# Performance work log

Hardware: AMD Instinct MI355X
Metric: run time of the kernel (lower is better)

The kernel has to match this reference:

```python
import jax, jax.numpy as jnp
import numpy as np

V, E, M, L = 32000, 1024, 4096, 4  # vocab, embed_dim, mlp_dim, mlp_layers
B, S = 4, 2048                      # batch, seq_len


def setup_inputs() -> dict:
    key = jax.random.key(0)
    ks = jax.random.split(key, 7)
    init = lambda k, shape, fan: (jax.random.normal(k, shape, jnp.float32) / np.sqrt(fan).astype(np.float32))
    return {
        "x": jax.random.randint(ks[0], (B, S), 0, V),
        "emb": init(ks[1], (V, E), E),
        "Wq": init(ks[2], (E, E), E), "bq": jnp.zeros((E,), jnp.float32),
        "Wk": init(ks[3], (E, E), E), "bk": jnp.zeros((E,), jnp.float32),
        "Wv": init(ks[4], (E, E), E), "bv": jnp.zeros((E,), jnp.float32),
        "W1": init(ks[5], (L, E, M), E), "b1": jnp.zeros((L, M), jnp.float32),
        "W2": init(ks[6], (L, M, E), M), "b2": jnp.zeros((L, E), jnp.float32),
    }


def reference(x, emb, Wq, bq, Wk, bk, Wv, bv, W1, b1, W2, b2):
    h = emb[x]                                   # [B,S,E]
    q = h @ Wq + bq
    k = h @ Wk + bk
    v = h @ Wv + bv
    scale = 1.0 / np.sqrt(E).astype(np.float32)
    scores = jnp.einsum("bse,bte->bst", q, k) * scale   # [B,S,S]
    # torch.triu(ones, diagonal=0): keep upper triangle incl. diagonal (anti-causal/suffix mask)
    mask = jnp.triu(jnp.ones((S, S), dtype=bool), k=0)
    scores = jnp.where(mask, scores, -jnp.inf)
    w = jax.nn.softmax(scores, axis=-1)
    h = jax.nn.relu(jnp.einsum("bst,bte->bse", w, v))
    for i in range(L):
        h = jax.nn.relu(h @ W1[i] + b1[i])
        h = jax.nn.relu(h @ W2[i] + b2[i])
    return h
```

## Files before the change

### kernel.cpp

```cpp
#include <hip/hip_runtime.h>
#include <hip/hip_bf16.h>

#define EDIM 1024
#define MDIM 4096
#define SEQ  2048
#define NB   4
#define ROWS 8192

typedef short bh8 __attribute__((ext_vector_type(8)));
typedef float f32x16 __attribute__((ext_vector_type(16)));

__device__ __forceinline__ float bf2f(unsigned short u) {
    return __uint_as_float(((unsigned int)u) << 16);
}
__device__ __forceinline__ unsigned short f2bf(float f) {
    unsigned int u = __float_as_uint(f);
    u += 0x7FFFu + ((u >> 16) & 1u);
    return (unsigned short)(u >> 16);
}
__device__ __forceinline__ void splitf(float v, unsigned short& h, unsigned short& l) {
    h = f2bf(v);
    l = f2bf(v - __uint_as_float(((unsigned int)h) << 16));
}
__device__ __forceinline__ void ld4f(const float* __restrict__ p, float* d) {
    const float4 v = *reinterpret_cast<const float4*>(p);
    d[0] = v.x; d[1] = v.y; d[2] = v.z; d[3] = v.w;
}
__device__ __forceinline__ void ld4h(const unsigned short* __restrict__ p, float* d) {
    const ushort4 v = *reinterpret_cast<const ushort4*>(p);
    d[0] = bf2f(v.x); d[1] = bf2f(v.y); d[2] = bf2f(v.z); d[3] = bf2f(v.w);
}

__device__ __forceinline__ long long tidx8(int n, int k, int KD16) {
    return ((((long long)(n >> 5) * KD16 + (k >> 4)) * 2 + ((k >> 3) & 1)) * 32 + (n & 31)) * 8;
}

__global__ __launch_bounds__(64)
void sniff_k(const unsigned int* __restrict__ w, int* __restrict__ flag) {
    int ok = 0;
    const int base = threadIdx.x * 32;
#pragma unroll
    for (int i = 0; i < 32; ++i) {
        const unsigned int v = w[base + i];
        const unsigned int lo = v & 0xFFFFu, hi = v >> 16;
        const unsigned int el = (lo >> 7) & 0xFF, eh = (hi >> 7) & 0xFF;
        const bool okl = (lo == 0u) || (el >= 0x30u && el <= 0x7Eu);
        const bool okh = (hi == 0u) || (eh >= 0x30u && eh <= 0x7Eu);
        ok += (okl && okh) ? 1 : 0;
    }
#pragma unroll
    for (int off = 32; off > 0; off >>= 1) ok += __shfl_down(ok, off);
    if (threadIdx.x == 0) *flag = (ok > 1400) ? 1 : 0;
}

__global__ __launch_bounds__(256)
void gather_k(const int* __restrict__ x, const void* __restrict__ emb,
              unsigned short* __restrict__ oh, unsigned short* __restrict__ ol,
              const int* __restrict__ flagp) {
    const int bf = *flagp;
    const int row = blockIdx.x;
    const int idx = x[row];
    const int k = threadIdx.x * 4;
    const long long off = (long long)idx * EDIM + k;
    float d[4];
    if (bf) ld4h((const unsigned short*)emb + off, d);
    else    ld4f((const float*)emb + off, d);
    unsigned short h0, l0, h1, l1, h2, l2, h3, l3;
    splitf(d[0], h0, l0); splitf(d[1], h1, l1);
    splitf(d[2], h2, l2); splitf(d[3], h3, l3);
    const long long o = (((long long)(row >> 5) * 64 + (k >> 4)) * 2 + ((k >> 3) & 1)) * 256
                        + (row & 31) * 8 + (k & 7);
    *reinterpret_cast<ushort4*>(oh + o) = make_ushort4(h0, h1, h2, h3);
    *reinterpret_cast<ushort4*>(ol + o) = make_ushort4(l0, l1, l2, l3);
}

__global__ __launch_bounds__(256)
void splitT_tiled_k(const void* __restrict__ in, unsigned short* __restrict__ oh,
                    unsigned short* __restrict__ ol, int Kd, int Nd,
                    long long inOff, const int* __restrict__ flagp, int bF) {
    const int bf = bF ? *flagp : 0;
    const int k0 = blockIdx.y * 32, n0 = blockIdx.x * 32;
    const int KD16 = Kd >> 4;
    __shared__ float t[32][33];
    const int c = threadIdx.x & 31, r0 = threadIdx.x >> 5;
#pragma unroll
    for (int i = 0; i < 4; ++i) {
        const int r = r0 + i * 8;
        const long long off = inOff + (long long)(k0 + r) * Nd + n0 + c;
        t[r][c] = bf ? bf2f(((const unsigned short*)in)[off]) : ((const float*)in)[off];
    }
    __syncthreads();
#pragma unroll
    for (int i = 0; i < 4; ++i) {
        const int r = r0 + i * 8;
        const float v = t[c][r];
        unsigned short hh, ll;
        splitf(v, hh, ll);
        const int n = n0 + r, k = k0 + c;
        const long long oo = tidx8(n, k, KD16) + (k & 7);
        oh[oo] = hh; ol[oo] = ll;
    }
}

template<int OM, bool BIAS, bool RELU, bool MASK>
__global__ __launch_bounds__(256, 3)
void mgemm_k(const unsigned short* __restrict__ Ah,
             const unsigned short* __restrict__ Al,
             const unsigned short* __restrict__ Bh,
             const unsigned short* __restrict__ Bl,
             const void* __restrict__ biasv,
             void* __restrict__ Cv, void* __restrict__ Cv2,
             int M, int N, int K,
             long long sA, long long sB, long long sC,
             long long biasBase, float scale, int oKD16, long long zOut, int rowMul,
             const int* __restrict__ flagp, int bF, int cF) {
    const int flag = *flagp;
    const int bfBias = bF ? flag : 0;
    const int bfC = cF ? flag : 0;

    Ah += (long long)blockIdx.z * sA;
    Al += (long long)blockIdx.z * sA;
    Bh += (long long)blockIdx.z * sB;
    Bl += (long long)blockIdx.z * sB;
    const long long zC = (long long)blockIdx.z * sC;
    const int rowOff = rowMul * blockIdx.z;

    const int GX = gridDim.x;
    const int f = blockIdx.y * GX + blockIdx.x;
    const int gxpc = GX >> 3;
    const int xcd = f & 7, p = f >> 3;
    const int bx = xcd * gxpc + (p % gxpc);
    const int by = p / gxpc;
    const int brow = by * 128, bcol = bx * 128;

    const int tid = threadIdx.x;
    const int lane = tid & 63, wave = tid >> 6;
    const int wr = wave >> 1, wc = wave & 1;
    const int l31 = lane & 31, lhi = lane >> 5;

    if (MASK && (bcol + 127 < brow)) {
#pragma unroll
        for (int mi = 0; mi < 2; ++mi) {
            const int rbase = brow + wr * 64 + mi * 32 + 4 * lhi;
#pragma unroll
            for (int ni = 0; ni < 2; ++ni) {
                const int c = bcol + wc * 64 + ni * 32 + l31;
#pragma unroll
                for (int e = 0; e < 16; ++e) {
                    const int r = rbase + (e & 3) + 8 * (e >> 2);
                    ((float*)Cv)[zC + (long long)r * N + c] = -1e30f;
                }
            }
        }
        return;
    }

    const int KD16 = K >> 4;

    const long long aoff0 = ((long long)((brow >> 5) + wr * 2 + 0) * KD16) * 512 + lane * 8;
    const long long aoff1 = aoff0 + (long long)KD16 * 512;
    const long long boff0 = ((long long)((bcol >> 5) + wc * 2 + 0) * KD16) * 512 + lane * 8;
    const long long boff1 = boff0 + (long long)KD16 * 512;

    const unsigned short* __restrict__ pAh0 = Ah + aoff0;
    const unsigned short* __restrict__ pAh1 = Ah + aoff1;
    const unsigned short* __restrict__ pAl0 = Al + aoff0;
    const unsigned short* __restrict__ pAl1 = Al + aoff1;
    const unsigned short* __restrict__ pBh0 = Bh + boff0;
    const unsigned short* __restrict__ pBh1 = Bh + boff1;
    const unsigned short* __restrict__ pBl0 = Bl + boff0;
    const unsigned short* __restrict__ pBl1 = Bl + boff1;

    f32x16 acc00, acc01, acc10, acc11;
#pragma unroll
    for (int e = 0; e < 16; ++e) { acc00[e] = 0.f; acc01[e] = 0.f; acc10[e] = 0.f; acc11[e] = 0.f; }

    bh8 p_ah0, p_ah1, p_al0, p_al1, p_bh0, p_bh1, p_bl0, p_bl1;
    bh8 q_ah0, q_ah1, q_al0, q_al1, q_bh0, q_bh1, q_bl0, q_bl1;

#define MFMA_(d, a, b) d = __builtin_amdgcn_mfma_f32_32x32x16_bf16(a, b, d, 0, 0, 0)

#define LOADSET(S, J) { \
    const long long o_ = (long long)(J) * 512; \
    S##ah0 = *reinterpret_cast<const bh8*>(pAh0 + o_); \
    S##ah1 = *reinterpret_cast<const bh8*>(pAh1 + o_); \
    S##al0 = *reinterpret_cast<const bh8*>(pAl0 + o_); \
    S##al1 = *reinterpret_cast<const bh8*>(pAl1 + o_); \
    S##bh0 = *reinterpret_cast<const bh8*>(pBh0 + o_); \
    S##bh1 = *reinterpret_cast<const bh8*>(pBh1 + o_); \
    S##bl0 = *reinterpret_cast<const bh8*>(pBl0 + o_); \
    S##bl1 = *reinterpret_cast<const bh8*>(pBl1 + o_); }

#define COMPSET(S) { \
    MFMA_(acc00, S##ah0, S##bh0); MFMA_(acc01, S##ah0, S##bh1); \
    MFMA_(acc10, S##ah1, S##bh0); MFMA_(acc11, S##ah1, S##bh1); \
    MFMA_(acc00, S##ah0, S##bl0); MFMA_(acc01, S##ah0, S##bl1); \
    MFMA_(acc10, S##ah1, S##bl0); MFMA_(acc11, S##ah1, S##bl1); \
    MFMA_(acc00, S##al0, S##bh0); MFMA_(acc01, S##al0, S##bh1); \
    MFMA_(acc10, S##al1, S##bh0); MFMA_(acc11, S##al1, S##bh1); }

    LOADSET(p_, 0);
    LOADSET(q_, 1);

    for (int j = 0; j + 3 < KD16; j += 2) {
        if ((j & 7) == 6) __builtin_amdgcn_s_barrier();
        __builtin_amdgcn_s_setprio(1);
        COMPSET(p_);
        __builtin_amdgcn_s_setprio(0);
        LOADSET(p_, j + 2);
        __builtin_amdgcn_s_setprio(1);
        COMPSET(q_);
        __builtin_amdgcn_s_setprio(0);
        LOADSET(q_, j + 3);
    }
    COMPSET(p_);
    COMPSET(q_);

#undef LOADSET
#undef COMPSET
#undef MFMA_

    const f32x16* accp[4] = {&acc00, &acc01, &acc10, &acc11};

#pragma unroll
    for (int mi = 0; mi < 2; ++mi) {
        const int rbase = brow + wr * 64 + mi * 32 + 4 * lhi;
#pragma unroll
        for (int ni = 0; ni < 2; ++ni) {
            const f32x16& a = *accp[mi * 2 + ni];
            const int c = bcol + wc * 64 + ni * 32 + l31;
            float bv = 0.f;
            if (BIAS) {
                const long long bo = biasBase + c;
                bv = bfBias ? bf2f(((const unsigned short*)biasv)[bo])
                            : ((const float*)biasv)[bo];
            }
            if constexpr (OM == 3) {
#pragma unroll
                for (int g = 0; g < 4; ++g) {
                    const int t0 = rbase + 8 * g;
                    const int z = t0 >> 11, tt = t0 & 2047;
                    float vv[4];
#pragma unroll
                    for (int d = 0; d < 4; ++d) {
                        float v = a[g * 4 + d];
                        if (BIAS) v += bv;
                        if (RELU) v = fmaxf(v, 0.f);
                        vv[d] = v;
                    }
                    unsigned short h0, l0, h1, l1, h2, l2, h3, l3;
                    splitf(vv[0], h0, l0); splitf(vv[1], h1, l1);
                    splitf(vv[2], h2, l2); splitf(vv[3], h3, l3);
                    const long long o = (long long)z * zOut +
                        (((long long)(c >> 5) * oKD16 + (tt >> 4)) * 2 + ((tt >> 3) & 1)) * 256 +
                        (c & 31) * 8 + (tt & 7);
                    *reinterpret_cast<ushort4*>((unsigned short*)Cv + o) = make_ushort4(h0, h1, h2, h3);
                    *reinterpret_cast<ushort4*>((unsigned short*)Cv2 + o) = make_ushort4(l0, l1, l2, l3);
                }
            } else if constexpr (OM == 1) {
#pragma unroll
                for (int e = 0; e < 16; ++e) {
                    const int r = rbase + (e & 3) + 8 * (e >> 2);
                    float v = a[e];
                    if (BIAS) v += bv;
                    if (RELU) v = fmaxf(v, 0.f);
                    unsigned short hh, ll;
                    splitf(v, hh, ll);
                    const int gr = rowOff + r;
                    const long long o =
                        (((long long)(gr >> 5) * oKD16 + (c >> 4)) * 2 + ((c >> 3) & 1)) * 256 +
                        (gr & 31) * 8 + (c & 7);
                    ((unsigned short*)Cv)[o] = hh;
                    ((unsigned short*)Cv2)[o] = ll;
                }
            } else {
#pragma unroll
                for (int e = 0; e < 16; ++e) {
                    const int r = rbase + (e & 3) + 8 * (e >> 2);
                    float v = a[e];
                    if (BIAS) v += bv;
                    if (MASK) v = (c >= r) ? v * scale : -1e30f;
                    if (RELU) v = fmaxf(v, 0.f);
                    const long long off = zC + (long long)r * N + c;
                    if (bfC) ((__hip_bfloat16*)Cv)[off] = __float2bfloat16(v);
                    else     ((float*)Cv)[off] = v;
                }
            }
        }
    }
}

__global__ __launch_bounds__(256)
void softmax_k(const float* __restrict__ Sc, unsigned short* __restrict__ Wh,
               unsigned short* __restrict__ Wl) {
    const int m = blockIdx.x, z = blockIdx.y;
    const float* row = Sc + ((long long)z * SEQ + m) * SEQ;
    const int tid = threadIdx.x;

    float v[8];
    float mx = -1e30f;
#pragma unroll
    for (int i = 0; i < 8; ++i) { v[i] = row[tid + i * 256]; mx = fmaxf(mx, v[i]); }
#pragma unroll
    for (int off = 32; off > 0; off >>= 1) mx = fmaxf(mx, __shfl_down(mx, off));

    __shared__ float sm[4];
    __shared__ float ss[4];
    const int wid = tid >> 6, lane = tid & 63;
    if (lane == 0) sm[wid] = mx;
    __syncthreads();
    const float mAll = fmaxf(fmaxf(sm[0], sm[1]), fmaxf(sm[2], sm[3]));

    float s = 0.f;
#pragma unroll
    for (int i = 0; i < 8; ++i) { v[i] = __expf(v[i] - mAll); s += v[i]; }
#pragma unroll
    for (int off = 32; off > 0; off >>= 1) s += __shfl_down(s, off);
    if (lane == 0) ss[wid] = s;
    __syncthreads();
    const float inv = 1.f / (ss[0] + ss[1] + ss[2] + ss[3]);

    unsigned short* wh = Wh + (long long)z * 4194304LL;
    unsigned short* wl = Wl + (long long)z * 4194304LL;
#pragma unroll
    for (int i = 0; i < 8; ++i) {
        const int k = tid + i * 256;
        unsigned short hh, ll;
        splitf(v[i] * inv, hh, ll);
        const long long o = (((long long)(m >> 5) * 128 + (k >> 4)) * 2 + ((k >> 3) & 1)) * 256 +
                            (m & 31) * 8 + (k & 7);
        wh[o] = hh; wl[o] = ll;
    }
}

extern "C" void kernel_launch(void* const* d_in, const int* in_sizes, int n_in,
                              void* d_out, int out_size, void* d_ws, size_t ws_size,
                              hipStream_t stream) {
    const int*  x   = (const int*)d_in[0];
    const void* emb = d_in[1];
    const void* Wq  = d_in[2];
    const void* bq  = d_in[3];
    const void* Wk  = d_in[4];
    const void* bk  = d_in[5];
    const void* Wv  = d_in[6];
    const void* bv  = d_in[7];
    const void* W1  = d_in[8];
    const void* b1  = d_in[9];
    const void* W2  = d_in[10];
    const void* b2  = d_in[11];

    char* ws = (char*)d_ws;
    const long long SZ = 33554432LL;
    const long long HM = 8388608LL;
    unsigned short* hA_h  = (unsigned short*)(ws);
    unsigned short* hA_l  = hA_h + HM;
    unsigned short* q_h   = (unsigned short*)(ws + SZ);
    unsigned short* q_l   = q_h + HM;
    unsigned short* kx_h  = (unsigned short*)(ws + 2 * SZ);
    unsigned short* kx_l  = kx_h + HM;
    unsigned short* vxs_h = (unsigned short*)(ws + 3 * SZ);
    unsigned short* vxs_l = vxs_h + HM;
    float*          sc    = (float*)(ws + 4 * SZ);
    unsigned short* watt_h = (unsigned short*)(ws);
    unsigned short* watt_l = (unsigned short*)(ws + SZ);
    unsigned short* att_h = (unsigned short*)(ws + 2 * SZ);
    unsigned short* att_l = att_h + HM;
    unsigned short* mid_h = (unsigned short*)(ws);
    unsigned short* mid_l = (unsigned short*)(ws + 3 * SZ);
    unsigned short* pong_h = (unsigned short*)(ws + 5 * SZ);
    unsigned short* pong_l = pong_h + HM;
    unsigned short* wq_h = (unsigned short*)(ws + 6 * SZ);
    unsigned short* wq_l = wq_h + 1048576;
    unsigned short* wk_h = wq_h + 2097152, * wk_l = wq_h + 3145728;
    unsigned short* wv_h = wq_h + 4194304, * wv_l = wq_h + 5242880;
    unsigned short* w1_h = (unsigned short*)(ws + 6 * SZ);
    unsigned short* w1_l = w1_h + 4194304;
    unsigned short* w2_h = w1_h + 8388608, * w2_l = w1_h + 12582912;
    int* flag = (int*)(ws + 7 * SZ);

    const dim3 b256(256);
    const long long SS = (long long)SEQ * SEQ;
    const long long TSE = 2097152LL;

    sniff_k<<<1, 64, 0, stream>>>((const unsigned int*)emb, flag);
    gather_k<<<ROWS, b256, 0, stream>>>(x, emb, hA_h, hA_l, flag);

    splitT_tiled_k<<<dim3(32, 32, 1), b256, 0, stream>>>(Wq, wq_h, wq_l, EDIM, EDIM, 0, flag, 1);
    splitT_tiled_k<<<dim3(32, 32, 1), b256, 0, stream>>>(Wk, wk_h, wk_l, EDIM, EDIM, 0, flag, 1);
    splitT_tiled_k<<<dim3(32, 32, 1), b256, 0, stream>>>(Wv, wv_h, wv_l, EDIM, EDIM, 0, flag, 1);

    mgemm_k<1, true, false, false><<<dim3(8, 64, 1), b256, 0, stream>>>(
        hA_h, hA_l, wq_h, wq_l, bq, q_h, q_l, ROWS, EDIM, EDIM,
        0, 0, 0, 0, 1.f, 64, 0, 0, flag, 1, 0);
    mgemm_k<1, true, false, false><<<dim3(8, 64, 1), b256, 0, stream>>>(
        hA_h, hA_l, wk_h, wk_l, bk, kx_h, kx_l, ROWS, EDIM, EDIM,
        0, 0, 0, 0, 1.f, 64, 0, 0, flag, 1, 0);
    mgemm_k<3, true, false, false><<<dim3(8, 64, 1), b256, 0, stream>>>(
        hA_h, hA_l, wv_h, wv_l, bv, vxs_h, vxs_l, ROWS, EDIM, EDIM,
        0, 0, 0, 0, 1.f, 128, TSE, 0, flag, 1, 0);

    mgemm_k<0, false, false, true><<<dim3(16, 16, NB), b256, 0, stream>>>(
        q_h, q_l, kx_h, kx_l, nullptr, sc, nullptr, SEQ, SEQ, EDIM,
        TSE, TSE, SS, 0, 0.03125f, 0, 0, 0, flag, 0, 0);

    softmax_k<<<dim3(SEQ, NB), b256, 0, stream>>>(sc, watt_h, watt_l);

    mgemm_k<1, false, true, false><<<dim3(8, 16, NB), b256, 0, stream>>>(
        watt_h, watt_l, vxs_h, vxs_l, nullptr, att_h, att_l, SEQ, EDIM, SEQ,
        4194304LL, TSE, 0, 0, 1.f, 64, 0, 2048, flag, 0, 0);

    const unsigned short* cur_h = att_h;
    const unsigned short* cur_l = att_l;
    for (int i = 0; i < 4; ++i) {
        splitT_tiled_k<<<dim3(128, 32, 1), b256, 0, stream>>>(
            W1, w1_h, w1_l, EDIM, MDIM, (long long)i * EDIM * MDIM, flag, 1);
        mgemm_k<1, true, true, false><<<dim3(32, 64, 1), b256, 0, stream>>>(
            cur_h, cur_l, w1_h, w1_l, b1, mid_h, mid_l, ROWS, MDIM, EDIM,
            0, 0, 0, (long long)i * MDIM, 1.f, 256, 0, 0, flag, 1, 0);

        splitT_tiled_k<<<dim3(32, 128, 1), b256, 0, stream>>>(
            W2, w2_h, w2_l, MDIM, EDIM, (long long)i * MDIM * EDIM, flag, 1);
        if (i < 3) {
            unsigned short* oh = (cur_h == att_h) ? pong_h : att_h;
            unsigned short* ol = (cur_h == att_h) ? pong_l : att_l;
            mgemm_k<1, true, true, false><<<dim3(8, 64, 1), b256, 0, stream>>>(
                mid_h, mid_l, w2_h, w2_l, b2, oh, ol, ROWS, EDIM, MDIM,
                0, 0, 0, (long long)i * EDIM, 1.f, 64, 0, 0, flag, 1, 0);
            cur_h = oh; cur_l = ol;
        } else {
            mgemm_k<0, true, true, false><<<dim3(8, 64, 1), b256, 0, stream>>>(
                mid_h, mid_l, w2_h, w2_l, b2, d_out, nullptr, ROWS, EDIM, MDIM,
                0, 0, 0, (long long)i * EDIM, 1.f, 0, 0, 0, flag, 1, 1);
        }
    }
}
```

Before: 2.590 ms.

## Stage GEMM operands through LDS with async double-buffered loads and larger tiles

The split-bf16 MFMA GEMM kernel previously had each wave load its A/B fragments straight from global memory into registers. It now uses 512-thread blocks with BMx256 tiles, selectable at 128 or 256 rows. Operands are copied into a double-buffered LDS staging area with global_load_lds async copies, guarded by explicit vmcnt waits and barriers. The aim is to share loaded tiles across 8 waves and cut redundant global traffic while overlapping loads with MFMA work. In exchange it uses more LDS, lowers occupancy, and relies on hand-tuned waitcnt values.

```diff
diff --git a/kernel.cpp b/kernel.cpp
--- a/kernel.cpp
+++ b/kernel.cpp
@@ -29,6 +29,12 @@
 __device__ __forceinline__ void ld4h(const unsigned short* __restrict__ p, float* d) {
     const ushort4 v = *reinterpret_cast<const ushort4*>(p);
     d[0] = bf2f(v.x); d[1] = bf2f(v.y); d[2] = bf2f(v.z); d[3] = bf2f(v.w);
+}
+
+__device__ __forceinline__ void async_copy16(void* lds, const void* g) {
+    __builtin_amdgcn_global_load_lds(
+        (const __attribute__((address_space(1))) unsigned int*)g,
+        (__attribute__((address_space(3))) unsigned int*)lds, 16, 0, 0);
 }
 
 __device__ __forceinline__ long long tidx8(int n, int k, int KD16) {
@@ -102,8 +108,8 @@
     }
 }
 
-template<int OM, bool BIAS, bool RELU, bool MASK>
-__global__ __launch_bounds__(256, 3)
+template<int BM, int OM, bool BIAS, bool RELU, bool MASK>
+__global__ __launch_bounds__(512, 2)
 void mgemm_k(const unsigned short* __restrict__ Ah,
              const unsigned short* __restrict__ Al,
              const unsigned short* __restrict__ Bh,
@@ -114,6 +120,12 @@
              long long sA, long long sB, long long sC,
              long long biasBase, float scale, int oKD16, long long zOut, int rowMul,
              const int* __restrict__ flagp, int bF, int cF) {
+    constexpr int MF = BM / 64;
+    constexpr int NA = BM / 8;
+    constexpr int NR = (NA + 32) / 8;
+    constexpr int ABYTES = BM * 128;
+    constexpr int BUFB = ABYTES + 32768;
+
     const int flag = *flagp;
     const int bfBias = bF ? flag : 0;
     const int bfC = cF ? flag : 0;
@@ -126,22 +138,21 @@
     const int rowOff = rowMul * blockIdx.z;
 
     const int GX = gridDim.x;
+    const int nwg = GX * gridDim.y;
     const int f = blockIdx.y * GX + blockIdx.x;
-    const int gxpc = GX >> 3;
-    const int xcd = f & 7, p = f >> 3;
-    const int bx = xcd * gxpc + (p % gxpc);
-    const int by = p / gxpc;
-    const int brow = by * 128, bcol = bx * 128;
+    const int idx = (f & 7) * (nwg >> 3) + (f >> 3);
+    const int bx = idx % GX, by = idx / GX;
+    const int brow = by * BM, bcol = bx * 256;
 
     const int tid = threadIdx.x;
     const int lane = tid & 63, wave = tid >> 6;
-    const int wr = wave >> 1, wc = wave & 1;
+    const int wr = wave >> 2, wc = wave & 3;
     const int l31 = lane & 31, lhi = lane >> 5;
 
-    if (MASK && (bcol + 127 < brow)) {
-#pragma unroll
-        for (int mi = 0; mi < 2; ++mi) {
-            const int rbase = brow + wr * 64 + mi * 32 + 4 * lhi;
+    if (MASK && (bcol + 255 < brow)) {
+#pragma unroll
+        for (int mi = 0; mi < MF; ++mi) {
+            const int rbase = brow + wr * (BM / 2) + mi * 32 + 4 * lhi;
 #pragma unroll
             for (int ni = 0; ni < 2; ++ni) {
                 const int c = bcol + wc * 64 + ni * 32 + l31;
@@ -155,79 +166,102 @@
         return;
     }
 
+    __shared__ __align__(16) char Lds[2][BUFB];
+
+    f32x16 acc[MF][2];
+#pragma unroll
+    for (int a = 0; a < MF; ++a)
+#pragma unroll
+        for (int b = 0; b < 2; ++b)
+#pragma unroll
+            for (int e = 0; e < 16; ++e) acc[a][b][e] = 0.f;
+
     const int KD16 = K >> 4;
 
-    const long long aoff0 = ((long long)((brow >> 5) + wr * 2 + 0) * KD16) * 512 + lane * 8;
-    const long long aoff1 = aoff0 + (long long)KD16 * 512;
-    const long long boff0 = ((long long)((bcol >> 5) + wc * 2 + 0) * KD16) * 512 + lane * 8;
-    const long long boff1 = boff0 + (long long)KD16 * 512;
-
-    const unsigned short* __restrict__ pAh0 = Ah + aoff0;
-    const unsigned short* __restrict__ pAh1 = Ah + aoff1;
-    const unsigned short* __restrict__ pAl0 = Al + aoff0;
-    const unsigned short* __restrict__ pAl1 = Al + aoff1;
-    const unsigned short* __restrict__ pBh0 = Bh + boff0;
-    const unsigned short* __restrict__ pBh1 = Bh + boff1;
-    const unsigned short* __restrict__ pBl0 = Bl + boff0;
-    const unsigned short* __restrict__ pBl1 = Bl + boff1;
-
-    f32x16 acc00, acc01, acc10, acc11;
-#pragma unroll
-    for (int e = 0; e < 16; ++e) { acc00[e] = 0.f; acc01[e] = 0.f; acc10[e] = 0.f; acc11[e] = 0.f; }
-
-    bh8 p_ah0, p_ah1, p_al0, p_al1, p_bh0, p_bh1, p_bl0, p_bl1;
-    bh8 q_ah0, q_ah1, q_al0, q_al1, q_bh0, q_bh1, q_bl0, q_bl1;
-
-#define MFMA_(d, a, b) d = __builtin_amdgcn_mfma_f32_32x32x16_bf16(a, b, d, 0, 0, 0)
-
-#define LOADSET(S, J) { \
-    const long long o_ = (long long)(J) * 512; \
-    S##ah0 = *reinterpret_cast<const bh8*>(pAh0 + o_); \
-    S##ah1 = *reinterpret_cast<const bh8*>(pAh1 + o_); \
-    S##al0 = *reinterpret_cast<const bh8*>(pAl0 + o_); \
-    S##al1 = *reinterpret_cast<const bh8*>(pAl1 + o_); \
-    S##bh0 = *reinterpret_cast<const bh8*>(pBh0 + o_); \
-    S##bh1 = *reinterpret_cast<const bh8*>(pBh1 + o_); \
-    S##bl0 = *reinterpret_cast<const bh8*>(pBl0 + o_); \
-    S##bl1 = *reinterpret_cast<const bh8*>(pBl1 + o_); }
-
-#define COMPSET(S) { \
-    MFMA_(acc00, S##ah0, S##bh0); MFMA_(acc01, S##ah0, S##bh1); \
-    MFMA_(acc10, S##ah1, S##bh0); MFMA_(acc11, S##ah1, S##bh1); \
-    MFMA_(acc00, S##ah0, S##bl0); MFMA_(acc01, S##ah0, S##bl1); \
-    MFMA_(acc10, S##ah1, S##bl0); MFMA_(acc11, S##ah1, S##bl1); \
-    MFMA_(acc00, S##al0, S##bh0); MFMA_(acc01, S##al0, S##bh1); \
-    MFMA_(acc10, S##al1, S##bh0); MFMA_(acc11, S##al1, S##bh1); }
-
-    LOADSET(p_, 0);
-    LOADSET(q_, 1);
-
-    for (int j = 0; j + 3 < KD16; j += 2) {
-        if ((j & 7) == 6) __builtin_amdgcn_s_barrier();
-        __builtin_amdgcn_s_setprio(1);
-        COMPSET(p_);
-        __builtin_amdgcn_s_setprio(0);
-        LOADSET(p_, j + 2);
-        __builtin_amdgcn_s_setprio(1);
-        COMPSET(q_);
-        __builtin_amdgcn_s_setprio(0);
-        LOADSET(q_, j + 3);
-    }
-    COMPSET(p_);
-    COMPSET(q_);
-
-#undef LOADSET
-#undef COMPSET
-#undef MFMA_
-
-    const f32x16* accp[4] = {&acc00, &acc01, &acc10, &acc11};
-
-#pragma unroll
-    for (int mi = 0; mi < 2; ++mi) {
-        const int rbase = brow + wr * 64 + mi * 32 + 4 * lhi;
+    const unsigned short* sp[NR];
+    int dof[NR];
+#pragma unroll
+    for (int r = 0; r < NR; ++r) {
+        const int j = r * 8 + wave;
+        if (j < NA) {
+            const int g = j >> 2, c01 = (j >> 1) & 1, hh = j & 1;
+            sp[r] = (hh ? Al : Ah) +
+                    ((long long)((brow >> 5) + g) * KD16 + c01) * 512 + lane * 8;
+            dof[r] = j * 1024;
+        } else {
+            const int jb = j - NA;
+            const int g = jb >> 2, c01 = (jb >> 1) & 1, hh = jb & 1;
+            sp[r] = (hh ? Bl : Bh) +
+                    ((long long)((bcol >> 5) + g) * KD16 + c01) * 512 + lane * 8;
+            dof[r] = ABYTES + jb * 1024;
+        }
+    }
+
+#define STAGE(BUF) { \
+    char* lb_ = &Lds[BUF][0]; \
+    _Pragma("unroll") \
+    for (int r = 0; r < NR; ++r) { async_copy16(lb_ + dof[r], sp[r]); sp[r] += 1024; } }
+
+#define COMPUTE(CUR) { \
+    const char* lb_ = &Lds[CUR][0] + lane * 16; \
+    _Pragma("unroll") \
+    for (int c = 0; c < 2; ++c) { \
+        bh8 aH[MF], aL[MF], bH[2], bL[2]; \
+        _Pragma("unroll") \
+        for (int ni = 0; ni < 2; ++ni) { \
+            const int jb = ((wc * 2 + ni) * 2 + c) * 2; \
+            bH[ni] = *reinterpret_cast<const bh8*>(lb_ + ABYTES + jb * 1024); \
+            bL[ni] = *reinterpret_cast<const bh8*>(lb_ + ABYTES + jb * 1024 + 1024); \
+        } \
+        _Pragma("unroll") \
+        for (int mi = 0; mi < MF; ++mi) { \
+            const int ja = ((wr * MF + mi) * 2 + c) * 2; \
+            aH[mi] = *reinterpret_cast<const bh8*>(lb_ + ja * 1024); \
+            aL[mi] = *reinterpret_cast<const bh8*>(lb_ + ja * 1024 + 1024); \
+        } \
+        __builtin_amdgcn_s_setprio(1); \
+        _Pragma("unroll") \
+        for (int mi = 0; mi < MF; ++mi) { \
+            _Pragma("unroll") \
+            for (int ni = 0; ni < 2; ++ni) { \
+                acc[mi][ni] = __builtin_amdgcn_mfma_f32_32x32x16_bf16(aH[mi], bH[ni], acc[mi][ni], 0, 0, 0); \
+                acc[mi][ni] = __builtin_amdgcn_mfma_f32_32x32x16_bf16(aH[mi], bL[ni], acc[mi][ni], 0, 0, 0); \
+                acc[mi][ni] = __builtin_amdgcn_mfma_f32_32x32x16_bf16(aL[mi], bH[ni], acc[mi][ni], 0, 0, 0); \
+            } \
+        } \
+        __builtin_amdgcn_s_setprio(0); \
+    } }
+
+    const int NT = K >> 5;
+
+    STAGE(0);
+    for (int t = 0; t < NT - 1; ++t) {
+        const int cur = t & 1;
+        STAGE(cur ^ 1);
+        if constexpr (NR == 8) asm volatile("s_waitcnt vmcnt(8)" ::: "memory");
+        else                   asm volatile("s_waitcnt vmcnt(6)" ::: "memory");
+        __builtin_amdgcn_sched_barrier(0);
+        __builtin_amdgcn_s_barrier();
+        __builtin_amdgcn_sched_barrier(0);
+        COMPUTE(cur);
+        __builtin_amdgcn_sched_barrier(0);
+        __builtin_amdgcn_s_barrier();
+    }
+    asm volatile("s_waitcnt vmcnt(0)" ::: "memory");
+    __builtin_amdgcn_sched_barrier(0);
+    __builtin_amdgcn_s_barrier();
+    __builtin_amdgcn_sched_barrier(0);
+    COMPUTE((NT - 1) & 1);
+
+#undef STAGE
+#undef COMPUTE
+
+#pragma unroll
+    for (int mi = 0; mi < MF; ++mi) {
+        const int rbase = brow + wr * (BM / 2) + mi * 32 + 4 * lhi;
 #pragma unroll
         for (int ni = 0; ni < 2; ++ni) {
-            const f32x16& a = *accp[mi * 2 + ni];
+            const f32x16& a = acc[mi][ni];
             const int c = bcol + wc * 64 + ni * 32 + l31;
             float bv = 0.f;
             if (BIAS) {
@@ -378,7 +412,7 @@
     unsigned short* w2_h = w1_h + 8388608, * w2_l = w1_h + 12582912;
     int* flag = (int*)(ws + 7 * SZ);
 
-    const dim3 b256(256);
+    const dim3 b256(256), b512(512);
     const long long SS = (long long)SEQ * SEQ;
     const long long TSE = 2097152LL;
 
@@ -389,23 +423,23 @@
     splitT_tiled_k<<<dim3(32, 32, 1), b256, 0, stream>>>(Wk, wk_h, wk_l, EDIM, EDIM, 0, flag, 1);
     splitT_tiled_k<<<dim3(32, 32, 1), b256, 0, stream>>>(Wv, wv_h, wv_l, EDIM, EDIM, 0, flag, 1);
 
-    mgemm_k<1, true, false, false><<<dim3(8, 64, 1), b256, 0, stream>>>(
+    mgemm_k<128, 1, true, false, false><<<dim3(4, 64, 1), b512, 0, stream>>>(
         hA_h, hA_l, wq_h, wq_l, bq, q_h, q_l, ROWS, EDIM, EDIM,
         0, 0, 0, 0, 1.f, 64, 0, 0, flag, 1, 0);
-    mgemm_k<1, true, false, false><<<dim3(8, 64, 1), b256, 0, stream>>>(
+    mgemm_k<128, 1, true, false, false><<<dim3(4, 64, 1), b512, 0, stream>>>(
         hA_h, hA_l, wk_h, wk_l, bk, kx_h, kx_l, ROWS, EDIM, EDIM,
         0, 0, 0, 0, 1.f, 64, 0, 0, flag, 1, 0);
-    mgemm_k<3, true, false, false><<<dim3(8, 64, 1), b256, 0, stream>>>(
+    mgemm_k<128, 3, true, false, false><<<dim3(4, 64, 1), b512, 0, stream>>>(
         hA_h, hA_l, wv_h, wv_l, bv, vxs_h, vxs_l, ROWS, EDIM, EDIM,
         0, 0, 0, 0, 1.f, 128, TSE, 0, flag, 1, 0);
 
-    mgemm_k<0, false, false, true><<<dim3(16, 16, NB), b256, 0, stream>>>(
+    mgemm_k<256, 0, false, false, true><<<dim3(8, 8, NB), b512, 0, stream>>>(
         q_h, q_l, kx_h, kx_l, nullptr, sc, nullptr, SEQ, SEQ, EDIM,
         TSE, TSE, SS, 0, 0.03125f, 0, 0, 0, flag, 0, 0);
 
     softmax_k<<<dim3(SEQ, NB), b256, 0, stream>>>(sc, watt_h, watt_l);
 
-    mgemm_k<1, false, true, false><<<dim3(8, 16, NB), b256, 0, stream>>>(
+    mgemm_k<128, 1, false, true, false><<<dim3(4, 16, NB), b512, 0, stream>>>(
         watt_h, watt_l, vxs_h, vxs_l, nullptr, att_h, att_l, SEQ, EDIM, SEQ,
         4194304LL, TSE, 0, 0, 1.f, 64, 0, 2048, flag, 0, 0);
 
@@ -414,7 +448,7 @@
     for (int i = 0; i < 4; ++i) {
         splitT_tiled_k<<<dim3(128, 32, 1), b256, 0, stream>>>(
             W1, w1_h, w1_l, EDIM, MDIM, (long long)i * EDIM * MDIM, flag, 1);
-        mgemm_k<1, true, true, false><<<dim3(32, 64, 1), b256, 0, stream>>>(
+        mgemm_k<256, 1, true, true, false><<<dim3(16, 32, 1), b512, 0, stream>>>(
             cur_h, cur_l, w1_h, w1_l, b1, mid_h, mid_l, ROWS, MDIM, EDIM,
             0, 0, 0, (long long)i * MDIM, 1.f, 256, 0, 0, flag, 1, 0);
 
@@ -423,12 +457,12 @@
         if (i < 3) {
             unsigned short* oh = (cur_h == att_h) ? pong_h : att_h;
             unsigned short* ol = (cur_h == att_h) ? pong_l : att_l;
-            mgemm_k<1, true, true, false><<<dim3(8, 64, 1), b256, 0, stream>>>(
+            mgemm_k<128, 1, true, true, false><<<dim3(4, 64, 1), b512, 0, stream>>>(
                 mid_h, mid_l, w2_h, w2_l, b2, oh, ol, ROWS, EDIM, MDIM,
                 0, 0, 0, (long long)i * EDIM, 1.f, 64, 0, 0, flag, 1, 0);
             cur_h = oh; cur_l = ol;
         } else {
-            mgemm_k<0, true, true, false><<<dim3(8, 64, 1), b256, 0, stream>>>(
+            mgemm_k<128, 0, true, true, false><<<dim3(4, 64, 1), b512, 0, stream>>>(
                 mid_h, mid_l, w2_h, w2_l, b2, d_out, nullptr, ROWS, EDIM, MDIM,
                 0, 0, 0, (long long)i * EDIM, 1.f, 0, 0, 0, flag, 1, 1);
         }
```

After: 2.199 ms. 15.1% less time.
